# Kernel tuning notes

Measured on AMD Instinct MI355X. Metric: run time of the kernel, lower is better.

Reference implementation:

```python
import jax, jax.numpy as jnp
import numpy as np

E, C, H, I = 8, 4096, 1024, 4096

def setup_inputs() -> dict:
    key = jax.random.key(0)
    k_x, k_g, k_u, k_d = jax.random.split(key, 4)
    scale_h = 1.0 / np.sqrt(H)
    scale_i = 1.0 / np.sqrt(I)
    return {
        "x_routed": jax.random.normal(k_x, (E, C, H), dtype=jnp.float32),
        "W_gate": jax.random.normal(k_g, (E, H, I), dtype=jnp.float32) * scale_h,
        "W_up": jax.random.normal(k_u, (E, H, I), dtype=jnp.float32) * scale_h,
        "W_down": jax.random.normal(k_d, (E, I, H), dtype=jnp.float32) * scale_i,
    }

def reference(x_routed, W_gate, W_up, W_down):
    # Per-expert SwiGLU MLP, batched over the expert axis as a grouped GEMM.
    # gate = silu(x @ Wg); up = x @ Wu; out = (gate * up) @ Wd
    gate = jax.nn.silu(jnp.einsum("ech,ehi->eci", x_routed, W_gate))
    up = jnp.einsum("ech,ehi->eci", x_routed, W_up)
    out = jnp.einsum("eci,eih->ech", gate * up, W_down)
    return out
```

## Files before the change

### kernel.cpp

```cpp
#include <hip/hip_runtime.h>
#include <hip/hip_bf16.h>
#include <stdint.h>
#include <stddef.h>

#define E_ 8
#define C_ 4096
#define H_ 1024
#define I_ 4096

typedef short s16;
typedef __attribute__((ext_vector_type(8))) short short8;
typedef __attribute__((ext_vector_type(4))) short short4v;
typedef __attribute__((ext_vector_type(4))) float f32x4;
typedef __attribute__((ext_vector_type(4))) float float4v;

__device__ __forceinline__ s16 f2bf(float f) {
  union { __hip_bfloat16 h; s16 s; } u;
  u.h = __float2bfloat16(f);
  return u.s;
}

__device__ __forceinline__ void gload16(const void* gsrc, void* ldst) {
  __builtin_amdgcn_global_load_lds(
      (const __attribute__((address_space(1))) void*)gsrc,
      (__attribute__((address_space(3))) void*)ldst, 16, 0, 0);
}

__global__ __launch_bounds__(256) void prep_kernel(
    const float* __restrict__ x, const float* __restrict__ Wg,
    const float* __restrict__ Wu, const float* __restrict__ Wd,
    s16* __restrict__ xb, s16* __restrict__ Wgu, s16* __restrict__ WdT)
{
  __shared__ float tile[64][65];
  const int t = threadIdx.x;
  const int z = blockIdx.z;
  const size_t e = blockIdx.y;

  if (z == 0) {
    size_t base = e * (size_t)C_ * H_ + ((size_t)blockIdx.x * 256 + t) * 16;
    for (int j = 0; j < 16; j += 8) {
      float4v v0 = *(const float4v*)(x + base + j);
      float4v v1 = *(const float4v*)(x + base + j + 4);
      s16 o[8];
      o[0] = f2bf(v0[0]); o[1] = f2bf(v0[1]); o[2] = f2bf(v0[2]); o[3] = f2bf(v0[3]);
      o[4] = f2bf(v1[0]); o[5] = f2bf(v1[1]); o[6] = f2bf(v1[2]); o[7] = f2bf(v1[3]);
      *(short8*)(xb + base + j) = *(short8*)o;
    }
    return;
  }

  const float* src; int Cc;
  if (z == 1)      { src = Wg + e * (size_t)H_ * I_; Cc = I_; }
  else if (z == 2) { src = Wu + e * (size_t)H_ * I_; Cc = I_; }
  else             { src = Wd + e * (size_t)H_ * I_; Cc = H_; }

  const int tpr  = Cc >> 6;
  const int trow = blockIdx.x / tpr;
  const int tcol = blockIdx.x % tpr;

  const int c = t & 63, rq = t >> 6;
  for (int i = 0; i < 16; ++i) {
    int r = rq * 16 + i;
    tile[r][c] = src[(size_t)(trow * 64 + r) * Cc + tcol * 64 + c];
  }
  __syncthreads();

  const int ro = t >> 2, cb = (t & 3) * 16;
  s16 o[16];
  for (int j = 0; j < 16; ++j) o[j] = f2bf(tile[cb + j][ro]);

  const int i0 = tcol * 64 + ro;
  s16* op;
  if (z == 3) {
    op = WdT + e * (size_t)H_ * I_ + (size_t)i0 * I_ + trow * 64 + cb;
  } else {
    int grow = ((i0 & ~15) << 1) + (i0 & 15) + ((z == 2) ? 16 : 0);
    op = Wgu + e * (size_t)2 * I_ * H_ + (size_t)grow * H_ + trow * 64 + cb;
  }
  *(short8*)op       = *(short8*)&o[0];
  *(short8*)(op + 8) = *(short8*)&o[8];
}

#define MFMA16(MH, A0, A1, A2, A3)                                                            \
  acc[(MH)*4+0][0] = __builtin_amdgcn_mfma_f32_16x16x32_bf16(bf[0], A0, acc[(MH)*4+0][0],0,0,0); \
  acc[(MH)*4+0][1] = __builtin_amdgcn_mfma_f32_16x16x32_bf16(bf[1], A0, acc[(MH)*4+0][1],0,0,0); \
  acc[(MH)*4+0][2] = __builtin_amdgcn_mfma_f32_16x16x32_bf16(bf[2], A0, acc[(MH)*4+0][2],0,0,0); \
  acc[(MH)*4+0][3] = __builtin_amdgcn_mfma_f32_16x16x32_bf16(bf[3], A0, acc[(MH)*4+0][3],0,0,0); \
  acc[(MH)*4+1][0] = __builtin_amdgcn_mfma_f32_16x16x32_bf16(bf[0], A1, acc[(MH)*4+1][0],0,0,0); \
  acc[(MH)*4+1][1] = __builtin_amdgcn_mfma_f32_16x16x32_bf16(bf[1], A1, acc[(MH)*4+1][1],0,0,0); \
  acc[(MH)*4+1][2] = __builtin_amdgcn_mfma_f32_16x16x32_bf16(bf[2], A1, acc[(MH)*4+1][2],0,0,0); \
  acc[(MH)*4+1][3] = __builtin_amdgcn_mfma_f32_16x16x32_bf16(bf[3], A1, acc[(MH)*4+1][3],0,0,0); \
  acc[(MH)*4+2][0] = __builtin_amdgcn_mfma_f32_16x16x32_bf16(bf[0], A2, acc[(MH)*4+2][0],0,0,0); \
  acc[(MH)*4+2][1] = __builtin_amdgcn_mfma_f32_16x16x32_bf16(bf[1], A2, acc[(MH)*4+2][1],0,0,0); \
  acc[(MH)*4+2][2] = __builtin_amdgcn_mfma_f32_16x16x32_bf16(bf[2], A2, acc[(MH)*4+2][2],0,0,0); \
  acc[(MH)*4+2][3] = __builtin_amdgcn_mfma_f32_16x16x32_bf16(bf[3], A2, acc[(MH)*4+2][3],0,0,0); \
  acc[(MH)*4+3][0] = __builtin_amdgcn_mfma_f32_16x16x32_bf16(bf[0], A3, acc[(MH)*4+3][0],0,0,0); \
  acc[(MH)*4+3][1] = __builtin_amdgcn_mfma_f32_16x16x32_bf16(bf[1], A3, acc[(MH)*4+3][1],0,0,0); \
  acc[(MH)*4+3][2] = __builtin_amdgcn_mfma_f32_16x16x32_bf16(bf[2], A3, acc[(MH)*4+3][2],0,0,0); \
  acc[(MH)*4+3][3] = __builtin_amdgcn_mfma_f32_16x16x32_bf16(bf[3], A3, acc[(MH)*4+3][3],0,0,0);

#define VMW4 asm volatile("s_waitcnt vmcnt(4)" ::: "memory");

#define LDAF(B, MH, M, CX) \
  (*(const short8*)(shm + (B)*16384 + ((wm + (MH)*64 + (M)*16 + lr) << 6) + (CX)))
#define LDBF(B, N, CX) \
  (*(const short8*)(shm + 32768 + (B)*16384 + ((wn + (N)*16 + lr) << 6) + (CX)))

#define PHASE(B, MH, CX, RDB, STMT, WV)                                      \
  {                                                                          \
    short8 af0 = LDAF(B, MH, 0, CX);                                         \
    short8 af1 = LDAF(B, MH, 1, CX);                                         \
    short8 af2 = LDAF(B, MH, 2, CX);                                         \
    short8 af3 = LDAF(B, MH, 3, CX);                                         \
    if (RDB) {                                                               \
      bf[0] = LDBF(B, 0, CX); bf[1] = LDBF(B, 1, CX);                        \
      bf[2] = LDBF(B, 2, CX); bf[3] = LDBF(B, 3, CX);                        \
    }                                                                        \
    STMT                                                                     \
    __builtin_amdgcn_sched_barrier(0);                                       \
    __builtin_amdgcn_s_barrier();                                            \
    asm volatile("s_waitcnt lgkmcnt(0)" ::: "memory");                       \
    __builtin_amdgcn_sched_barrier(0);                                       \
    __builtin_amdgcn_s_setprio(1);                                           \
    MFMA16(MH, af0, af1, af2, af3)                                           \
    __builtin_amdgcn_s_setprio(0);                                           \
    __builtin_amdgcn_sched_barrier(0);                                       \
    WV                                                                       \
    __builtin_amdgcn_s_barrier();                                            \
  }

__global__ __launch_bounds__(512, 2) void gemm_gu(
    const s16* __restrict__ Abase, const s16* __restrict__ Bbase,
    s16* __restrict__ HOut)
{
  constexpr int K  = H_;
  constexpr int NB = 2 * I_;
  constexpr int NT = K / 64;

  __shared__ s16 shm[65536];

  const int tid  = threadIdx.x;
  const int wave = tid >> 6, lane = tid & 63;
  const int e    = blockIdx.z;

  const int bid = blockIdx.x;
  const int xcd = bid & 7;
  const int idx = bid >> 3;
  const int bn = (xcd & 3) * 8 + (idx & 7);
  const int bm = (xcd >> 2) * 8 + (idx >> 3);

  const s16* A = Abase + (size_t)e * C_ * K + (size_t)bm * 256 * K;
  const s16* B = Bbase + (size_t)e * NB * K + (size_t)bn * 256 * K;

  const int wm  = (wave >> 2) * 128;
  const int wn  = (wave & 3) * 64;
  const int lr  = lane & 15;
  const int lkb = (lane >> 4) * 8;
  const int xr  = (lr & 7) << 3;
  const int cx0 = lkb ^ xr;
  const int cx1 = (32 + lkb) ^ xr;

  const int srow = tid >> 3;
  const int scol = ((tid & 7) ^ (srow & 7)) * 8;
  const size_t stoff = (size_t)srow * K + scol;
  const int sdst = wave * 512;

  auto stageA = [&](int kt, int b) {
    #pragma unroll
    for (int h = 0; h < 2; ++h)
      #pragma unroll
      for (int ll = 0; ll < 2; ++ll)
        gload16(A + (size_t)(h * 128 + ll * 64) * K + (size_t)kt * 64 + stoff,
                shm + b * 16384 + h * 8192 + ll * 4096 + sdst);
  };
  auto stageB = [&](int kt, int b) {
    #pragma unroll
    for (int h = 0; h < 2; ++h)
      #pragma unroll
      for (int ll = 0; ll < 2; ++ll)
        gload16(B + (size_t)(h * 128 + ll * 64) * K + (size_t)kt * 64 + stoff,
                shm + 32768 + b * 16384 + h * 8192 + ll * 4096 + sdst);
  };

  f32x4 acc[8][4];
  #pragma unroll
  for (int m = 0; m < 8; ++m)
    #pragma unroll
    for (int n = 0; n < 4; ++n) acc[m][n] = (f32x4){0.f, 0.f, 0.f, 0.f};

  stageB(0, 0);
  stageA(0, 0);
  stageB(1, 1);
  VMW4
  __builtin_amdgcn_sched_barrier(0);
  __builtin_amdgcn_s_barrier();

  short8 bf[4];
  for (int i = 0; i < NT / 2; ++i) {
    const int t1 = 2 * i + 1;
    const int t2 = (2 * i + 2 < NT) ? (2 * i + 2) : (NT - 1);
    const int t3 = (2 * i + 3 < NT) ? (2 * i + 3) : (NT - 1);
    PHASE(0, 0, cx0, 1, { stageA(t1, 1); }, )
    PHASE(0, 1, cx0, 0, {}, )
    PHASE(0, 0, cx1, 1, {}, )
    PHASE(0, 1, cx1, 0, { stageB(t2, 0); }, VMW4)
    PHASE(1, 0, cx0, 1, { stageA(t2, 0); }, )
    PHASE(1, 1, cx0, 0, {}, )
    PHASE(1, 0, cx1, 1, {}, )
    PHASE(1, 1, cx1, 0, { stageB(t3, 1); }, VMW4)
  }

  const int lcc = (lane >> 4) * 4;
  s16* Hp = HOut + (size_t)e * C_ * I_;
  const int ibase = bn * 128 + (wn >> 1);
  #pragma unroll
  for (int m = 0; m < 8; ++m) {
    const int row = bm * 256 + wm + m * 16 + lr;
    #pragma unroll
    for (int p = 0; p < 2; ++p) {
      const int col = ibase + p * 16 + lcc;
      s16 o4[4];
      #pragma unroll
      for (int q = 0; q < 4; ++q) {
        float g = acc[m][2 * p][q], u = acc[m][2 * p + 1][q];
        float sg = 1.0f / (1.0f + __expf(-g));
        o4[q] = f2bf(g * sg * u);
      }
      *(short4v*)(Hp + (size_t)row * I_ + col) = *(short4v*)o4;
    }
  }
}

__global__ __launch_bounds__(512, 2) void gemm_dn(
    const s16* __restrict__ Abase, const s16* __restrict__ Bbase,
    float* __restrict__ FOut)
{
  constexpr int K  = I_;
  constexpr int NB = H_;
  constexpr int NT = K / 64;
  constexpr int TN = NB / 256;
  constexpr int TM = C_ / 256;
  constexpr int NWG = TM * TN;

  __shared__ s16 shm[65536];

  const int tid  = threadIdx.x;
  const int wave = tid >> 6, lane = tid & 63;
  const int e    = blockIdx.z;

  const int bid = blockIdx.x;
  const int swz = (bid & 7) * (NWG / 8) + (bid >> 3);
  const int bm = swz / TN, bn = swz % TN;

  const s16* A = Abase + (size_t)e * C_ * K + (size_t)bm * 256 * K;
  const s16* B = Bbase + (size_t)e * NB * K + (size_t)bn * 256 * K;

  const int wm  = (wave >> 2) * 128;
  const int wn  = (wave & 3) * 64;
  const int lr  = lane & 15;
  const int lkb = (lane >> 4) * 8;
  const int xr  = (lr & 7) << 3;
  const int cx0 = lkb ^ xr;
  const int cx1 = (32 + lkb) ^ xr;

  const int srow = tid >> 3;
  const int scol = ((tid & 7) ^ (srow & 7)) * 8;
  const size_t stoff = (size_t)srow * K + scol;
  const int sdst = wave * 512;

  auto stageA = [&](int kt, int b) {
    #pragma unroll
    for (int h = 0; h < 2; ++h)
      #pragma unroll
      for (int ll = 0; ll < 2; ++ll)
        gload16(A + (size_t)(h * 128 + ll * 64) * K + (size_t)kt * 64 + stoff,
                shm + b * 16384 + h * 8192 + ll * 4096 + sdst);
  };
  auto stageB = [&](int kt, int b) {
    #pragma unroll
    for (int h = 0; h < 2; ++h)
      #pragma unroll
      for (int ll = 0; ll < 2; ++ll)
        gload16(B + (size_t)(h * 128 + ll * 64) * K + (size_t)kt * 64 + stoff,
                shm + 32768 + b * 16384 + h * 8192 + ll * 4096 + sdst);
  };

  f32x4 acc[8][4];
  #pragma unroll
  for (int m = 0; m < 8; ++m)
    #pragma unroll
    for (int n = 0; n < 4; ++n) acc[m][n] = (f32x4){0.f, 0.f, 0.f, 0.f};

  stageB(0, 0);
  stageA(0, 0);
  stageB(1, 1);
  VMW4
  __builtin_amdgcn_sched_barrier(0);
  __builtin_amdgcn_s_barrier();

  short8 bf[4];
  for (int i = 0; i < NT / 2; ++i) {
    const int t1 = 2 * i + 1;
    const int t2 = (2 * i + 2 < NT) ? (2 * i + 2) : (NT - 1);
    const int t3 = (2 * i + 3 < NT) ? (2 * i + 3) : (NT - 1);
    PHASE(0, 0, cx0, 1, { stageA(t1, 1); }, )
    PHASE(0, 1, cx0, 0, {}, )
    PHASE(0, 0, cx1, 1, {}, )
    PHASE(0, 1, cx1, 0, { stageB(t2, 0); }, VMW4)
    PHASE(1, 0, cx0, 1, { stageA(t2, 0); }, )
    PHASE(1, 1, cx0, 0, {}, )
    PHASE(1, 0, cx1, 1, {}, )
    PHASE(1, 1, cx1, 0, { stageB(t3, 1); }, VMW4)
  }

  const int lcc = (lane >> 4) * 4;
  float* Op = FOut + (size_t)e * C_ * H_;
  #pragma unroll
  for (int m = 0; m < 8; ++m) {
    const int row = bm * 256 + wm + m * 16 + lr;
    #pragma unroll
    for (int n = 0; n < 4; ++n) {
      const int col = bn * 256 + wn + n * 16 + lcc;
      *(float4v*)(Op + (size_t)row * H_ + col) = acc[m][n];
    }
  }
}

extern "C" void kernel_launch(void* const* d_in, const int* in_sizes, int n_in,
                              void* d_out, int out_size, void* d_ws, size_t ws_size,
                              hipStream_t stream) {
  const float* x  = (const float*)d_in[0];
  const float* Wg = (const float*)d_in[1];
  const float* Wu = (const float*)d_in[2];
  const float* Wd = (const float*)d_in[3];
  float* out = (float*)d_out;

  const size_t szX  = (size_t)C_ * H_;
  const size_t szGU = (size_t)2 * I_ * H_;
  const size_t szWd = (size_t)H_ * I_;
  const size_t szH  = (size_t)C_ * I_;

  const size_t needFull = 2 * E_ * (szX + szGU + szWd + szH);

  constexpr int GU_BLK = (C_ / 256) * (2 * I_ / 256);
  constexpr int DN_BLK = (C_ / 256) * (H_ / 256);

  if (ws_size >= needFull) {
    s16* xb  = (s16*)d_ws;
    s16* Wgu = xb  + E_ * szX;
    s16* WdT = Wgu + E_ * szGU;
    s16* hbf = WdT + E_ * szWd;

    prep_kernel<<<dim3(1024, E_, 4), 256, 0, stream>>>(
        x, Wg, Wu, Wd, xb, Wgu, WdT);
    gemm_gu<<<dim3(GU_BLK, 1, E_), 512, 0, stream>>>(
        xb, Wgu, hbf);
    gemm_dn<<<dim3(DN_BLK, 1, E_), 512, 0, stream>>>(
        hbf, WdT, out);
  } else {
    s16* xb  = (s16*)d_ws;
    s16* Wgu = xb  + szX;
    s16* WdT = Wgu + szGU;
    s16* hbf = WdT + szWd;

    for (int e = 0; e < E_; ++e) {
      prep_kernel<<<dim3(1024, 1, 4), 256, 0, stream>>>(
          x + e * szX, Wg + e * szWd, Wu + e * szWd, Wd + e * szWd,
          xb, Wgu, WdT);
      gemm_gu<<<dim3(GU_BLK, 1, 1), 512, 0, stream>>>(
          xb, Wgu, hbf);
      gemm_dn<<<dim3(DN_BLK, 1, 1), 512, 0, stream>>>(
          hbf, WdT, out + e * szX);
    }
  }
}
```

Measured before the change: 958.3 us.

## Switch both GEMMs to 32x32x16 MFMA with fragment-major LDS layout

Replaces the 16x16x32 bf16 MFMA tiles with 32x32x16 MFMA in both the gate/up and down GEMMs. Staging now writes LDS in a fragment-major order so each lane reads its operand with a single contiguous 16-byte load. This drops the XOR swizzle and halves the number of barrier phases per k-tile. The aim is fewer MFMA issues and LDS reads per flop, in exchange for rewritten epilogue index mapping (including the gate/up interleave) that must match the new accumulator layout, plus possibly strided global loads.

```diff
diff --git a/kernel.cpp b/kernel.cpp
--- a/kernel.cpp
+++ b/kernel.cpp
@@ -11,7 +11,7 @@
 typedef short s16;
 typedef __attribute__((ext_vector_type(8))) short short8;
 typedef __attribute__((ext_vector_type(4))) short short4v;
-typedef __attribute__((ext_vector_type(4))) float f32x4;
+typedef __attribute__((ext_vector_type(16))) float f32x16;
 typedef __attribute__((ext_vector_type(4))) float float4v;
 
 __device__ __forceinline__ s16 f2bf(float f) {
@@ -81,51 +81,46 @@
   *(short8*)(op + 8) = *(short8*)&o[8];
 }
 
-#define MFMA16(MH, A0, A1, A2, A3)                                                            \
-  acc[(MH)*4+0][0] = __builtin_amdgcn_mfma_f32_16x16x32_bf16(bf[0], A0, acc[(MH)*4+0][0],0,0,0); \
-  acc[(MH)*4+0][1] = __builtin_amdgcn_mfma_f32_16x16x32_bf16(bf[1], A0, acc[(MH)*4+0][1],0,0,0); \
-  acc[(MH)*4+0][2] = __builtin_amdgcn_mfma_f32_16x16x32_bf16(bf[2], A0, acc[(MH)*4+0][2],0,0,0); \
-  acc[(MH)*4+0][3] = __builtin_amdgcn_mfma_f32_16x16x32_bf16(bf[3], A0, acc[(MH)*4+0][3],0,0,0); \
-  acc[(MH)*4+1][0] = __builtin_amdgcn_mfma_f32_16x16x32_bf16(bf[0], A1, acc[(MH)*4+1][0],0,0,0); \
-  acc[(MH)*4+1][1] = __builtin_amdgcn_mfma_f32_16x16x32_bf16(bf[1], A1, acc[(MH)*4+1][1],0,0,0); \
-  acc[(MH)*4+1][2] = __builtin_amdgcn_mfma_f32_16x16x32_bf16(bf[2], A1, acc[(MH)*4+1][2],0,0,0); \
-  acc[(MH)*4+1][3] = __builtin_amdgcn_mfma_f32_16x16x32_bf16(bf[3], A1, acc[(MH)*4+1][3],0,0,0); \
-  acc[(MH)*4+2][0] = __builtin_amdgcn_mfma_f32_16x16x32_bf16(bf[0], A2, acc[(MH)*4+2][0],0,0,0); \
-  acc[(MH)*4+2][1] = __builtin_amdgcn_mfma_f32_16x16x32_bf16(bf[1], A2, acc[(MH)*4+2][1],0,0,0); \
-  acc[(MH)*4+2][2] = __builtin_amdgcn_mfma_f32_16x16x32_bf16(bf[2], A2, acc[(MH)*4+2][2],0,0,0); \
-  acc[(MH)*4+2][3] = __builtin_amdgcn_mfma_f32_16x16x32_bf16(bf[3], A2, acc[(MH)*4+2][3],0,0,0); \
-  acc[(MH)*4+3][0] = __builtin_amdgcn_mfma_f32_16x16x32_bf16(bf[0], A3, acc[(MH)*4+3][0],0,0,0); \
-  acc[(MH)*4+3][1] = __builtin_amdgcn_mfma_f32_16x16x32_bf16(bf[1], A3, acc[(MH)*4+3][1],0,0,0); \
-  acc[(MH)*4+3][2] = __builtin_amdgcn_mfma_f32_16x16x32_bf16(bf[2], A3, acc[(MH)*4+3][2],0,0,0); \
-  acc[(MH)*4+3][3] = __builtin_amdgcn_mfma_f32_16x16x32_bf16(bf[3], A3, acc[(MH)*4+3][3],0,0,0);
-
 #define VMW4 asm volatile("s_waitcnt vmcnt(4)" ::: "memory");
 
-#define LDAF(B, MH, M, CX) \
-  (*(const short8*)(shm + (B)*16384 + ((wm + (MH)*64 + (M)*16 + lr) << 6) + (CX)))
-#define LDBF(B, N, CX) \
-  (*(const short8*)(shm + 32768 + (B)*16384 + ((wn + (N)*16 + lr) << 6) + (CX)))
-
-#define PHASE(B, MH, CX, RDB, STMT, WV)                                      \
+#define LDA32(B, KS, MF) \
+  (*(const short8*)(shm + (B)*16384 + (KS)*4096 + (aR + (MF))*512 + l8))
+#define LDB32(B, KS, NF) \
+  (*(const short8*)(shm + 32768 + (B)*16384 + (KS)*4096 + (bR + (NF))*512 + l8))
+
+#define PHASE32(B, KS, TOPSTMT, TAILSTMT)                                    \
   {                                                                          \
-    short8 af0 = LDAF(B, MH, 0, CX);                                         \
-    short8 af1 = LDAF(B, MH, 1, CX);                                         \
-    short8 af2 = LDAF(B, MH, 2, CX);                                         \
-    short8 af3 = LDAF(B, MH, 3, CX);                                         \
-    if (RDB) {                                                               \
-      bf[0] = LDBF(B, 0, CX); bf[1] = LDBF(B, 1, CX);                        \
-      bf[2] = LDBF(B, 2, CX); bf[3] = LDBF(B, 3, CX);                        \
-    }                                                                        \
-    STMT                                                                     \
+    short8 a00 = LDA32(B, (KS),   0), a01 = LDA32(B, (KS),   1);             \
+    short8 a02 = LDA32(B, (KS),   2), a03 = LDA32(B, (KS),   3);             \
+    short8 a10 = LDA32(B, (KS)+1, 0), a11 = LDA32(B, (KS)+1, 1);             \
+    short8 a12 = LDA32(B, (KS)+1, 2), a13 = LDA32(B, (KS)+1, 3);             \
+    short8 b00 = LDB32(B, (KS),   0), b01 = LDB32(B, (KS),   1);             \
+    short8 b10 = LDB32(B, (KS)+1, 0), b11 = LDB32(B, (KS)+1, 1);             \
+    TOPSTMT                                                                  \
     __builtin_amdgcn_sched_barrier(0);                                       \
     __builtin_amdgcn_s_barrier();                                            \
     asm volatile("s_waitcnt lgkmcnt(0)" ::: "memory");                       \
     __builtin_amdgcn_sched_barrier(0);                                       \
     __builtin_amdgcn_s_setprio(1);                                           \
-    MFMA16(MH, af0, af1, af2, af3)                                           \
+    acc[0][0] = __builtin_amdgcn_mfma_f32_32x32x16_bf16(b00, a00, acc[0][0], 0, 0, 0); \
+    acc[0][1] = __builtin_amdgcn_mfma_f32_32x32x16_bf16(b01, a00, acc[0][1], 0, 0, 0); \
+    acc[1][0] = __builtin_amdgcn_mfma_f32_32x32x16_bf16(b00, a01, acc[1][0], 0, 0, 0); \
+    acc[1][1] = __builtin_amdgcn_mfma_f32_32x32x16_bf16(b01, a01, acc[1][1], 0, 0, 0); \
+    acc[2][0] = __builtin_amdgcn_mfma_f32_32x32x16_bf16(b00, a02, acc[2][0], 0, 0, 0); \
+    acc[2][1] = __builtin_amdgcn_mfma_f32_32x32x16_bf16(b01, a02, acc[2][1], 0, 0, 0); \
+    acc[3][0] = __builtin_amdgcn_mfma_f32_32x32x16_bf16(b00, a03, acc[3][0], 0, 0, 0); \
+    acc[3][1] = __builtin_amdgcn_mfma_f32_32x32x16_bf16(b01, a03, acc[3][1], 0, 0, 0); \
+    acc[0][0] = __builtin_amdgcn_mfma_f32_32x32x16_bf16(b10, a10, acc[0][0], 0, 0, 0); \
+    acc[0][1] = __builtin_amdgcn_mfma_f32_32x32x16_bf16(b11, a10, acc[0][1], 0, 0, 0); \
+    acc[1][0] = __builtin_amdgcn_mfma_f32_32x32x16_bf16(b10, a11, acc[1][0], 0, 0, 0); \
+    acc[1][1] = __builtin_amdgcn_mfma_f32_32x32x16_bf16(b11, a11, acc[1][1], 0, 0, 0); \
+    acc[2][0] = __builtin_amdgcn_mfma_f32_32x32x16_bf16(b10, a12, acc[2][0], 0, 0, 0); \
+    acc[2][1] = __builtin_amdgcn_mfma_f32_32x32x16_bf16(b11, a12, acc[2][1], 0, 0, 0); \
+    acc[3][0] = __builtin_amdgcn_mfma_f32_32x32x16_bf16(b10, a13, acc[3][0], 0, 0, 0); \
+    acc[3][1] = __builtin_amdgcn_mfma_f32_32x32x16_bf16(b11, a13, acc[3][1], 0, 0, 0); \
     __builtin_amdgcn_s_setprio(0);                                           \
     __builtin_amdgcn_sched_barrier(0);                                       \
-    WV                                                                       \
+    TAILSTMT                                                                 \
     __builtin_amdgcn_s_barrier();                                            \
   }
 
@@ -152,41 +147,34 @@
   const s16* A = Abase + (size_t)e * C_ * K + (size_t)bm * 256 * K;
   const s16* B = Bbase + (size_t)e * NB * K + (size_t)bn * 256 * K;
 
-  const int wm  = (wave >> 2) * 128;
-  const int wn  = (wave & 3) * 64;
-  const int lr  = lane & 15;
-  const int lkb = (lane >> 4) * 8;
-  const int xr  = (lr & 7) << 3;
-  const int cx0 = lkb ^ xr;
-  const int cx1 = (32 + lkb) ^ xr;
-
-  const int srow = tid >> 3;
-  const int scol = ((tid & 7) ^ (srow & 7)) * 8;
-  const size_t stoff = (size_t)srow * K + scol;
-  const int sdst = wave * 512;
+  const int wm = (wave >> 2) * 128;
+  const int wn = (wave & 3) * 64;
+  const int aR = (wave >> 2) * 4;
+  const int bR = (wave & 3) * 2;
+  const int l8 = lane * 8;
+  const int lrow = lane & 31;
+  const int lkg  = (lane >> 5) * 8;
 
   auto stageA = [&](int kt, int b) {
     #pragma unroll
-    for (int h = 0; h < 2; ++h)
-      #pragma unroll
-      for (int ll = 0; ll < 2; ++ll)
-        gload16(A + (size_t)(h * 128 + ll * 64) * K + (size_t)kt * 64 + stoff,
-                shm + b * 16384 + h * 8192 + ll * 4096 + sdst);
+    for (int i = 0; i < 4; ++i)
+      gload16(A + (size_t)(wave * 32 + lrow) * K + kt * 64 + i * 16 + lkg,
+              shm + b * 16384 + i * 4096 + wave * 512);
   };
   auto stageB = [&](int kt, int b) {
     #pragma unroll
-    for (int h = 0; h < 2; ++h)
+    for (int i = 0; i < 4; ++i)
+      gload16(B + (size_t)(wave * 32 + lrow) * K + kt * 64 + i * 16 + lkg,
+              shm + 32768 + b * 16384 + i * 4096 + wave * 512);
+  };
+
+  f32x16 acc[4][2];
+  #pragma unroll
+  for (int m = 0; m < 4; ++m)
+    #pragma unroll
+    for (int n = 0; n < 2; ++n)
       #pragma unroll
-      for (int ll = 0; ll < 2; ++ll)
-        gload16(B + (size_t)(h * 128 + ll * 64) * K + (size_t)kt * 64 + stoff,
-                shm + 32768 + b * 16384 + h * 8192 + ll * 4096 + sdst);
-  };
-
-  f32x4 acc[8][4];
-  #pragma unroll
-  for (int m = 0; m < 8; ++m)
-    #pragma unroll
-    for (int n = 0; n < 4; ++n) acc[m][n] = (f32x4){0.f, 0.f, 0.f, 0.f};
+      for (int q = 0; q < 16; ++q) acc[m][n][q] = 0.f;
 
   stageB(0, 0);
   stageA(0, 0);
@@ -195,38 +183,37 @@
   __builtin_amdgcn_sched_barrier(0);
   __builtin_amdgcn_s_barrier();
 
-  short8 bf[4];
   for (int i = 0; i < NT / 2; ++i) {
     const int t1 = 2 * i + 1;
     const int t2 = (2 * i + 2 < NT) ? (2 * i + 2) : (NT - 1);
     const int t3 = (2 * i + 3 < NT) ? (2 * i + 3) : (NT - 1);
-    PHASE(0, 0, cx0, 1, { stageA(t1, 1); }, )
-    PHASE(0, 1, cx0, 0, {}, )
-    PHASE(0, 0, cx1, 1, {}, )
-    PHASE(0, 1, cx1, 0, { stageB(t2, 0); }, VMW4)
-    PHASE(1, 0, cx0, 1, { stageA(t2, 0); }, )
-    PHASE(1, 1, cx0, 0, {}, )
-    PHASE(1, 0, cx1, 1, {}, )
-    PHASE(1, 1, cx1, 0, { stageB(t3, 1); }, VMW4)
-  }
-
-  const int lcc = (lane >> 4) * 4;
+    PHASE32(0, 0, { stageA(t1, 1); }, )
+    PHASE32(0, 2, {}, { stageB(t2, 0); VMW4 })
+    PHASE32(1, 0, { stageA(t2, 0); }, )
+    PHASE32(1, 2, {}, { stageB(t3, 1); VMW4 })
+  }
+
   s16* Hp = HOut + (size_t)e * C_ * I_;
-  const int ibase = bn * 128 + (wn >> 1);
+  const int ib0 = bn * 128 + (wn >> 1);
+  const int lkh4 = (lane >> 5) * 4;
   #pragma unroll
-  for (int m = 0; m < 8; ++m) {
-    const int row = bm * 256 + wm + m * 16 + lr;
-    #pragma unroll
-    for (int p = 0; p < 2; ++p) {
-      const int col = ibase + p * 16 + lcc;
-      s16 o4[4];
+  for (int MF = 0; MF < 4; ++MF) {
+    const int row = bm * 256 + wm + MF * 32 + lrow;
+    #pragma unroll
+    for (int NF = 0; NF < 2; ++NF) {
       #pragma unroll
-      for (int q = 0; q < 4; ++q) {
-        float g = acc[m][2 * p][q], u = acc[m][2 * p + 1][q];
-        float sg = 1.0f / (1.0f + __expf(-g));
-        o4[q] = f2bf(g * sg * u);
+      for (int q = 0; q < 2; ++q) {
+        const int col = ib0 + NF * 16 + q * 8 + lkh4;
+        s16 o4[4];
+        #pragma unroll
+        for (int j = 0; j < 4; ++j) {
+          float g = acc[MF][NF][4 * q + j];
+          float u = acc[MF][NF][8 + 4 * q + j];
+          float sg = 1.0f / (1.0f + __expf(-g));
+          o4[j] = f2bf(g * sg * u);
+        }
+        *(short4v*)(Hp + (size_t)row * I_ + col) = *(short4v*)o4;
       }
-      *(short4v*)(Hp + (size_t)row * I_ + col) = *(short4v*)o4;
     }
   }
 }
@@ -255,41 +242,34 @@
   const s16* A = Abase + (size_t)e * C_ * K + (size_t)bm * 256 * K;
   const s16* B = Bbase + (size_t)e * NB * K + (size_t)bn * 256 * K;
 
-  const int wm  = (wave >> 2) * 128;
-  const int wn  = (wave & 3) * 64;
-  const int lr  = lane & 15;
-  const int lkb = (lane >> 4) * 8;
-  const int xr  = (lr & 7) << 3;
-  const int cx0 = lkb ^ xr;
-  const int cx1 = (32 + lkb) ^ xr;
-
-  const int srow = tid >> 3;
-  const int scol = ((tid & 7) ^ (srow & 7)) * 8;
-  const size_t stoff = (size_t)srow * K + scol;
-  const int sdst = wave * 512;
+  const int wm = (wave >> 2) * 128;
+  const int wn = (wave & 3) * 64;
+  const int aR = (wave >> 2) * 4;
+  const int bR = (wave & 3) * 2;
+  const int l8 = lane * 8;
+  const int lrow = lane & 31;
+  const int lkg  = (lane >> 5) * 8;
 
   auto stageA = [&](int kt, int b) {
     #pragma unroll
-    for (int h = 0; h < 2; ++h)
-      #pragma unroll
-      for (int ll = 0; ll < 2; ++ll)
-        gload16(A + (size_t)(h * 128 + ll * 64) * K + (size_t)kt * 64 + stoff,
-                shm + b * 16384 + h * 8192 + ll * 4096 + sdst);
+    for (int i = 0; i < 4; ++i)
+      gload16(A + (size_t)(wave * 32 + lrow) * K + kt * 64 + i * 16 + lkg,
+              shm + b * 16384 + i * 4096 + wave * 512);
   };
   auto stageB = [&](int kt, int b) {
     #pragma unroll
-    for (int h = 0; h < 2; ++h)
+    for (int i = 0; i < 4; ++i)
+      gload16(B + (size_t)(wave * 32 + lrow) * K + kt * 64 + i * 16 + lkg,
+              shm + 32768 + b * 16384 + i * 4096 + wave * 512);
+  };
+
+  f32x16 acc[4][2];
+  #pragma unroll
+  for (int m = 0; m < 4; ++m)
+    #pragma unroll
+    for (int n = 0; n < 2; ++n)
       #pragma unroll
-      for (int ll = 0; ll < 2; ++ll)
-        gload16(B + (size_t)(h * 128 + ll * 64) * K + (size_t)kt * 64 + stoff,
-                shm + 32768 + b * 16384 + h * 8192 + ll * 4096 + sdst);
-  };
-
-  f32x4 acc[8][4];
-  #pragma unroll
-  for (int m = 0; m < 8; ++m)
-    #pragma unroll
-    for (int n = 0; n < 4; ++n) acc[m][n] = (f32x4){0.f, 0.f, 0.f, 0.f};
+      for (int q = 0; q < 16; ++q) acc[m][n][q] = 0.f;
 
   stageB(0, 0);
   stageA(0, 0);
@@ -298,30 +278,33 @@
   __builtin_amdgcn_sched_barrier(0);
   __builtin_amdgcn_s_barrier();
 
-  short8 bf[4];
   for (int i = 0; i < NT / 2; ++i) {
     const int t1 = 2 * i + 1;
     const int t2 = (2 * i + 2 < NT) ? (2 * i + 2) : (NT - 1);
     const int t3 = (2 * i + 3 < NT) ? (2 * i + 3) : (NT - 1);
-    PHASE(0, 0, cx0, 1, { stageA(t1, 1); }, )
-    PHASE(0, 1, cx0, 0, {}, )
-    PHASE(0, 0, cx1, 1, {}, )
-    PHASE(0, 1, cx1, 0, { stageB(t2, 0); }, VMW4)
-    PHASE(1, 0, cx0, 1, { stageA(t2, 0); }, )
-    PHASE(1, 1, cx0, 0, {}, )
-    PHASE(1, 0, cx1, 1, {}, )
-    PHASE(1, 1, cx1, 0, { stageB(t3, 1); }, VMW4)
-  }
-
-  const int lcc = (lane >> 4) * 4;
+    PHASE32(0, 0, { stageA(t1, 1); }, )
+    PHASE32(0, 2, {}, { stageB(t2, 0); VMW4 })
+    PHASE32(1, 0, { stageA(t2, 0); }, )
+    PHASE32(1, 2, {}, { stageB(t3, 1); VMW4 })
+  }
+
   float* Op = FOut + (size_t)e * C_ * H_;
+  const int lkh4 = (lane >> 5) * 4;
   #pragma unroll
-  for (int m = 0; m < 8; ++m) {
-    const int row = bm * 256 + wm + m * 16 + lr;
-    #pragma unroll
-    for (int n = 0; n < 4; ++n) {
-      const int col = bn * 256 + wn + n * 16 + lcc;
-      *(float4v*)(Op + (size_t)row * H_ + col) = acc[m][n];
+  for (int MF = 0; MF < 4; ++MF) {
+    const int row = bm * 256 + wm + MF * 32 + lrow;
+    #pragma unroll
+    for (int NF = 0; NF < 2; ++NF) {
+      #pragma unroll
+      for (int q = 0; q < 4; ++q) {
+        const int col = bn * 256 + wn + NF * 32 + q * 8 + lkh4;
+        float4v v;
+        v[0] = acc[MF][NF][4 * q + 0];
+        v[1] = acc[MF][NF][4 * q + 1];
+        v[2] = acc[MF][NF][4 * q + 2];
+        v[3] = acc[MF][NF][4 * q + 3];
+        *(float4v*)(Op + (size_t)row * H_ + col) = v;
+      }
     }
   }
 }
```

After: 1.282 ms. 33.8% more time.
